# Kernel tuning notes

Measured on AMD Instinct MI355X. Metric: run time of the kernel, lower is better.

Reference implementation:

```python
import jax, jax.numpy as jnp
import numpy as np

BN_EPS = 1e-5

def _ste_sign(x):
    # forward: sign in {-1,+1}; backward: clipped straight-through (grad 1 on [-1,1])
    s = jnp.where(x >= 0, 1.0, -1.0).astype(x.dtype)
    c = jnp.clip(x, -1.0, 1.0)
    return c + jax.lax.stop_gradient(s - c)

def setup_inputs() -> dict:
    key = jax.random.key(0)
    ks = jax.random.split(key, 8)
    N, C, H, W = 32, 256, 56, 56
    x = jax.random.normal(ks[0], (N, C, H, W), dtype=jnp.float32)
    bias0 = jax.random.normal(ks[1], (C,), dtype=jnp.float32) * 0.1
    w = jax.random.normal(ks[2], (C, C, 1, 1), dtype=jnp.float32) * 0.05
    gamma = jnp.ones((C,), dtype=jnp.float32)
    beta = jnp.zeros((C,), dtype=jnp.float32)
    bias1 = jax.random.normal(ks[3], (C,), dtype=jnp.float32) * 0.1
    alpha = jnp.full((C,), 0.25, dtype=jnp.float32)  # PReLU init
    bias2 = jax.random.normal(ks[4], (C,), dtype=jnp.float32) * 0.1
    return {"x": x, "bias0": bias0, "w": w, "gamma": gamma, "beta": beta,
            "bias1": bias1, "alpha": alpha, "bias2": bias2}

def reference(x, bias0, w, gamma, beta, bias1, alpha, bias2):
    ch = lambda v: v[None, :, None, None]
    # move0: learnable per-channel bias
    out = x + ch(bias0)
    # binary activation: sign (STE)
    out = _ste_sign(out)
    # binarized 1x1 conv: w_bin = mean(|w|) per out-channel * sign(w)
    scale = jnp.mean(jnp.abs(w), axis=(1, 2, 3))              # [O]
    wb = scale[:, None] * _ste_sign(w[:, :, 0, 0])            # [O, C]
    out = jnp.einsum('nchw,oc->nohw', out, wb)                # 1x1 conv
    # bn1: batch statistics (training-mode math)
    mu = jnp.mean(out, axis=(0, 2, 3), keepdims=True)
    var = jnp.var(out, axis=(0, 2, 3), keepdims=True)
    out = ch(gamma) * (out - mu) * jax.lax.rsqrt(var + BN_EPS) + ch(beta)
    # residual add (downsample is None)
    out = out + x
    # move1 -> PReLU -> move2
    out = out + ch(bias1)
    out = jnp.where(out > 0, out, ch(alpha) * out)
    out = out + ch(bias2)
    return out
```

## Files before the change

kernel.cpp:

```cpp
#include <hip/hip_runtime.h>
#include <stdint.h>

typedef unsigned long long u64;
typedef unsigned int u32;
typedef float f32x2 __attribute__((ext_vector_type(2)));
typedef float f32x4 __attribute__((ext_vector_type(4)));

constexpr int kC  = 256;
constexpr int kHW = 3136;
constexpr int kN  = 32;
constexpr int kP  = kN * kHW;
constexpr int kPos = 128;
constexpr int kBlk = kP / kPos;
constexpr int kRedBlk  = 16;
constexpr int kRedRows = kBlk / kRedBlk;

constexpr size_t OFF_T     = 0;
constexpr size_t OFF_SCALE = 8192;
constexpr size_t OFF_SUMD  = 9216;
constexpr size_t OFF_SUMD2 = 11264;
constexpr size_t OFF_CC    = 13312;
constexpr size_t OFF_PS    = 17408;
constexpr size_t OFF_PQ    = 820224;
constexpr size_t OFF_D     = 1623040;

struct alignas(16) U64x2 { u64 x, y; };

__global__ __launch_bounds__(256) void prep_kernel(
    const float* __restrict__ w, char* __restrict__ ws) {
  int t = threadIdx.x;
  int b = blockIdx.x;
  u64*   T4    = (u64*)(ws + OFF_T);
  float* scale = (float*)(ws + OFF_SCALE);
  int kk = t >> 6, ln = t & 63;
  if (b == 0) {
    ((u64*)(ws + OFF_SUMD))[t]  = 0ull;
    ((u64*)(ws + OFF_SUMD2))[t] = 0ull;
  }
  __shared__ float part[4][16];
#pragma unroll
  for (int i = 0; i < 16; ++i) {
    int o = b * 16 + i;
    float v = w[o * kC + kk * 64 + ln];
    u64 m = __ballot(v >= 0.0f);
    float a = fabsf(v);
#pragma unroll
    for (int s = 32; s > 0; s >>= 1) a += __shfl_xor(a, s, 64);
    if (ln == 0) { T4[o * 4 + kk] = m; part[kk][i] = a; }
  }
  __syncthreads();
  if (t < 16) {
    int o = b * 16 + t;
    scale[o] = (part[0][t] + part[1][t] + part[2][t] + part[3][t]) * (1.0f / 256.0f);
  }
}

__global__ __launch_bounds__(256) void pack_d_kernel(
    const float* __restrict__ x, const float* __restrict__ bias0,
    char* __restrict__ ws) {
  __shared__ U64x2 tile[4][64];
  int t = threadIdx.x;
  int k    = __builtin_amdgcn_readfirstlane(t >> 6);
  int lane = t & 63;
  u32 pb = (u32)blockIdx.x * (u32)kPos;
  u32 p0 = pb + 2u * (u32)lane;
  u32 n  = p0 / kHW;
  u32 hw = p0 - n * kHW;
  const float* xp = x + (size_t)(n * kC + k * 64) * kHW + hw;
  const float* bp = bias0 + k * 64;

  u64 m0 = 0, m1 = 0;
#pragma unroll 8
  for (int i = 0; i < 64; ++i) {
    f32x2 v = *(const f32x2*)(xp + (size_t)i * kHW);
    float bc = bp[i];
    m0 |= (u64)(v.x + bc >= 0.0f) << i;
    m1 |= (u64)(v.y + bc >= 0.0f) << i;
  }
  U64x2 mm; mm.x = m0; mm.y = m1;
  tile[k][lane] = mm;
  __syncthreads();

  U64x2 sa = tile[0][lane], sb = tile[1][lane],
        sc = tile[2][lane], sd = tile[3][lane];

  const u64* T4 = (const u64*)(ws + OFF_T);
  u32* D = (u32*)(ws + OFF_D);
  int myPS = 0, myPQ = 0;
#pragma unroll 4
  for (int i = 0; i < 64; ++i) {
    int o = k * 64 + i;
    u64 t0 = T4[4 * o], t1 = T4[4 * o + 1], t2 = T4[4 * o + 2], t3 = T4[4 * o + 3];
    int q0 = __popcll(sa.x ^ t0) + __popcll(sb.x ^ t1) +
             __popcll(sc.x ^ t2) + __popcll(sd.x ^ t3);
    int q1 = __popcll(sa.y ^ t0) + __popcll(sb.y ^ t1) +
             __popcll(sc.y ^ t2) + __popcll(sd.y ^ t3);
    D[(size_t)o * (kP / 2) + (pb >> 1) + lane] = (u32)q0 | ((u32)q1 << 16);
    int a0 = 128 - q0, a1 = 128 - q1;
    int s  = a0 + a1;
    int sq = a0 * a0 + a1 * a1;
#pragma unroll
    for (int msk = 1; msk < 64; msk <<= 1) {
      s  += __shfl_xor(s,  msk, 64);
      sq += __shfl_xor(sq, msk, 64);
    }
    if (lane == i) { myPS = s; myPQ = sq; }
  }
  ((int*)(ws + OFF_PS))[blockIdx.x * 256 + t] = myPS;
  ((int*)(ws + OFF_PQ))[blockIdx.x * 256 + t] = myPQ;
}

__global__ __launch_bounds__(256) void reduce_kernel(char* __restrict__ ws) {
  int t = threadIdx.x;
  int b = blockIdx.x;
  const int* PS = (const int*)(ws + OFF_PS);
  const int* PQ = (const int*)(ws + OFF_PQ);
  long long s = 0, q = 0;
#pragma unroll 7
  for (int r = 0; r < kRedRows; ++r) {
    int row = b * kRedRows + r;
    s += PS[row * 256 + t];
    q += PQ[row * 256 + t];
  }
  atomicAdd((u64*)(ws + OFF_SUMD) + t,  (u64)(long long)(2 * s));
  atomicAdd((u64*)(ws + OFF_SUMD2) + t, (u64)(long long)(4 * q));
}

__global__ __launch_bounds__(256) void coef_kernel(
    const float* __restrict__ gamma, const float* __restrict__ beta,
    const float* __restrict__ bias1, const float* __restrict__ alpha,
    const float* __restrict__ bias2, char* __restrict__ ws) {
  int t = threadIdx.x;
  const float*     scale = (const float*)(ws + OFF_SCALE);
  const long long* sumd  = (const long long*)(ws + OFF_SUMD);
  const long long* sumd2 = (const long long*)(ws + OFF_SUMD2);
  double inv  = 1.0 / (double)kP;
  double md   = (double)sumd[t] * inv;
  double e2   = (double)sumd2[t] * inv;
  double vard = e2 - md * md;
  float sc  = scale[t];
  float mu  = sc * (float)md;
  float var = sc * sc * (float)vard;
  float rs  = rsqrtf(var + 1e-5f);
  float g   = gamma[t];
  float cA  = g * rs * sc;
  float cB  = beta[t] - g * rs * mu + bias1[t];
  f32x4 cc; cc.x = 2.0f * cA; cc.y = cB; cc.z = alpha[t]; cc.w = bias2[t];
  ((f32x4*)(ws + OFF_CC))[t] = cc;
}

__global__ __launch_bounds__(256) void finalize_kernel(
    const float* __restrict__ x, const char* __restrict__ ws,
    float* __restrict__ out) {
  int t = threadIdx.x;
  int k    = __builtin_amdgcn_readfirstlane(t >> 6);
  int lane = t & 63;
  u32 pb = (u32)blockIdx.x * (u32)kPos;
  u32 p0 = pb + 2u * (u32)lane;
  u32 n  = p0 / kHW;
  u32 hw = p0 - n * kHW;

  const float* xp = x   + (size_t)(n * kC + k * 64) * kHW + hw;
  float*       op = out + (size_t)(n * kC + k * 64) * kHW + hw;
  const u32*   D  = (const u32*)(ws + OFF_D);
  const f32x4* CC = (const f32x4*)(ws + OFF_CC);
  u32 dbase = (pb >> 1) + (u32)lane;

#pragma unroll 4
  for (int i = 0; i < 64; ++i) {
    int o = k * 64 + i;
    f32x4 cc = CC[o];
    u32 d = D[(size_t)o * (kP / 2) + dbase];
    f32x2 xv = *(const f32x2*)(xp + (size_t)i * kHW);
    float u0 = fmaf(cc.x, (float)(128 - (int)(d & 0xFFFFu)), cc.y) + xv.x;
    float u1 = fmaf(cc.x, (float)(128 - (int)(d >> 16)),     cc.y) + xv.y;
    f32x2 r;
    r.x = (u0 > 0.0f ? u0 : cc.z * u0) + cc.w;
    r.y = (u1 > 0.0f ? u1 : cc.z * u1) + cc.w;
    __builtin_nontemporal_store(r, (f32x2*)(op + (size_t)i * kHW));
  }
}

extern "C" void kernel_launch(void* const* d_in, const int* in_sizes, int n_in,
                              void* d_out, int out_size, void* d_ws, size_t ws_size,
                              hipStream_t stream) {
  const float* x     = (const float*)d_in[0];
  const float* bias0 = (const float*)d_in[1];
  const float* w     = (const float*)d_in[2];
  const float* gamma = (const float*)d_in[3];
  const float* beta  = (const float*)d_in[4];
  const float* bias1 = (const float*)d_in[5];
  const float* alpha = (const float*)d_in[6];
  const float* bias2 = (const float*)d_in[7];
  float* out = (float*)d_out;
  char*  ws  = (char*)d_ws;

  hipLaunchKernelGGL(prep_kernel, dim3(16), dim3(256), 0, stream, w, ws);
  hipLaunchKernelGGL(pack_d_kernel, dim3(kBlk), dim3(256), 0, stream,
                     x, bias0, ws);
  hipLaunchKernelGGL(reduce_kernel, dim3(kRedBlk), dim3(256), 0, stream, ws);
  hipLaunchKernelGGL(coef_kernel, dim3(1), dim3(256), 0, stream,
                     gamma, beta, bias1, alpha, bias2, ws);
  hipLaunchKernelGGL(finalize_kernel, dim3(kBlk), dim3(256), 0, stream,
                     x, ws, out);
}
```

Measured before the change: 273.4 us.

## Compute BN stats by rereading packed D per channel; drop shuffle reductions

```diff
diff --git a/kernel.cpp b/kernel.cpp
--- a/kernel.cpp
+++ b/kernel.cpp
@@ -12,16 +12,12 @@
 constexpr int kP  = kN * kHW;
 constexpr int kPos = 128;
 constexpr int kBlk = kP / kPos;
-constexpr int kRedBlk  = 16;
-constexpr int kRedRows = kBlk / kRedBlk;
+constexpr int kDW  = kP / 2;
+constexpr int kStIt = kDW / 256;
 
 constexpr size_t OFF_T     = 0;
 constexpr size_t OFF_SCALE = 8192;
-constexpr size_t OFF_SUMD  = 9216;
-constexpr size_t OFF_SUMD2 = 11264;
 constexpr size_t OFF_CC    = 13312;
-constexpr size_t OFF_PS    = 17408;
-constexpr size_t OFF_PQ    = 820224;
 constexpr size_t OFF_D     = 1623040;
 
 struct alignas(16) U64x2 { u64 x, y; };
@@ -33,10 +29,6 @@
   u64*   T4    = (u64*)(ws + OFF_T);
   float* scale = (float*)(ws + OFF_SCALE);
   int kk = t >> 6, ln = t & 63;
-  if (b == 0) {
-    ((u64*)(ws + OFF_SUMD))[t]  = 0ull;
-    ((u64*)(ws + OFF_SUMD2))[t] = 0ull;
-  }
   __shared__ float part[4][16];
 #pragma unroll
   for (int i = 0; i < 16; ++i) {
@@ -86,8 +78,8 @@
 
   const u64* T4 = (const u64*)(ws + OFF_T);
   u32* D = (u32*)(ws + OFF_D);
-  int myPS = 0, myPQ = 0;
-#pragma unroll 4
+  u32 dbase = (pb >> 1) + (u32)lane;
+#pragma unroll 8
   for (int i = 0; i < 64; ++i) {
     int o = k * 64 + i;
     u64 t0 = T4[4 * o], t1 = T4[4 * o + 1], t2 = T4[4 * o + 2], t3 = T4[4 * o + 3];
@@ -95,58 +87,53 @@
              __popcll(sc.x ^ t2) + __popcll(sd.x ^ t3);
     int q1 = __popcll(sa.y ^ t0) + __popcll(sb.y ^ t1) +
              __popcll(sc.y ^ t2) + __popcll(sd.y ^ t3);
-    D[(size_t)o * (kP / 2) + (pb >> 1) + lane] = (u32)q0 | ((u32)q1 << 16);
-    int a0 = 128 - q0, a1 = 128 - q1;
-    int s  = a0 + a1;
-    int sq = a0 * a0 + a1 * a1;
-#pragma unroll
-    for (int msk = 1; msk < 64; msk <<= 1) {
-      s  += __shfl_xor(s,  msk, 64);
-      sq += __shfl_xor(sq, msk, 64);
-    }
-    if (lane == i) { myPS = s; myPQ = sq; }
+    D[(size_t)o * kDW + dbase] = (u32)q0 | ((u32)q1 << 16);
   }
-  ((int*)(ws + OFF_PS))[blockIdx.x * 256 + t] = myPS;
-  ((int*)(ws + OFF_PQ))[blockIdx.x * 256 + t] = myPQ;
 }
 
-__global__ __launch_bounds__(256) void reduce_kernel(char* __restrict__ ws) {
-  int t = threadIdx.x;
-  int b = blockIdx.x;
-  const int* PS = (const int*)(ws + OFF_PS);
-  const int* PQ = (const int*)(ws + OFF_PQ);
-  long long s = 0, q = 0;
-#pragma unroll 7
-  for (int r = 0; r < kRedRows; ++r) {
-    int row = b * kRedRows + r;
-    s += PS[row * 256 + t];
-    q += PQ[row * 256 + t];
-  }
-  atomicAdd((u64*)(ws + OFF_SUMD) + t,  (u64)(long long)(2 * s));
-  atomicAdd((u64*)(ws + OFF_SUMD2) + t, (u64)(long long)(4 * q));
-}
-
-__global__ __launch_bounds__(256) void coef_kernel(
+__global__ __launch_bounds__(256) void stats_coef_kernel(
     const float* __restrict__ gamma, const float* __restrict__ beta,
     const float* __restrict__ bias1, const float* __restrict__ alpha,
     const float* __restrict__ bias2, char* __restrict__ ws) {
   int t = threadIdx.x;
-  const float*     scale = (const float*)(ws + OFF_SCALE);
-  const long long* sumd  = (const long long*)(ws + OFF_SUMD);
-  const long long* sumd2 = (const long long*)(ws + OFF_SUMD2);
-  double inv  = 1.0 / (double)kP;
-  double md   = (double)sumd[t] * inv;
-  double e2   = (double)sumd2[t] * inv;
-  double vard = e2 - md * md;
-  float sc  = scale[t];
-  float mu  = sc * (float)md;
-  float var = sc * sc * (float)vard;
-  float rs  = rsqrtf(var + 1e-5f);
-  float g   = gamma[t];
-  float cA  = g * rs * sc;
-  float cB  = beta[t] - g * rs * mu + bias1[t];
-  f32x4 cc; cc.x = 2.0f * cA; cc.y = cB; cc.z = alpha[t]; cc.w = bias2[t];
-  ((f32x4*)(ws + OFF_CC))[t] = cc;
+  int o = blockIdx.x;
+  int wid = t >> 6, lane = t & 63;
+  const u32* Do = (const u32*)(ws + OFF_D) + (size_t)o * kDW;
+
+  int s = 0, sq = 0;
+#pragma unroll 14
+  for (int j = 0; j < kStIt; ++j) {
+    u32 d = Do[j * 256 + t];
+    int a0 = 128 - (int)(d & 0xFFFFu);
+    int a1 = 128 - (int)(d >> 16);
+    s  += a0 + a1;
+    sq += a0 * a0 + a1 * a1;
+  }
+#pragma unroll
+  for (int m = 32; m > 0; m >>= 1) {
+    s  += __shfl_down(s,  m, 64);
+    sq += __shfl_down(sq, m, 64);
+  }
+  __shared__ long long wsS[4], wsQ[4];
+  if (lane == 0) { wsS[wid] = s; wsQ[wid] = sq; }
+  __syncthreads();
+  if (t == 0) {
+    long long S  = wsS[0] + wsS[1] + wsS[2] + wsS[3];
+    long long SQ = wsQ[0] + wsQ[1] + wsQ[2] + wsQ[3];
+    double inv  = 1.0 / (double)kP;
+    double md   = (double)(2ll * S) * inv;
+    double e2   = (double)(4ll * SQ) * inv;
+    double vard = e2 - md * md;
+    float sc  = ((const float*)(ws + OFF_SCALE))[o];
+    float mu  = sc * (float)md;
+    float var = sc * sc * (float)vard;
+    float rs  = rsqrtf(var + 1e-5f);
+    float g   = gamma[o];
+    float cA  = g * rs * sc;
+    float cB  = beta[o] - g * rs * mu + bias1[o];
+    f32x4 cc; cc.x = 2.0f * cA; cc.y = cB; cc.z = alpha[o]; cc.w = bias2[o];
+    ((f32x4*)(ws + OFF_CC))[o] = cc;
+  }
 }
 
 __global__ __launch_bounds__(256) void finalize_kernel(
@@ -170,7 +157,7 @@
   for (int i = 0; i < 64; ++i) {
     int o = k * 64 + i;
     f32x4 cc = CC[o];
-    u32 d = D[(size_t)o * (kP / 2) + dbase];
+    u32 d = D[(size_t)o * kDW + dbase];
     f32x2 xv = *(const f32x2*)(xp + (size_t)i * kHW);
     float u0 = fmaf(cc.x, (float)(128 - (int)(d & 0xFFFFu)), cc.y) + xv.x;
     float u1 = fmaf(cc.x, (float)(128 - (int)(d >> 16)),     cc.y) + xv.y;
@@ -198,8 +185,7 @@
   hipLaunchKernelGGL(prep_kernel, dim3(16), dim3(256), 0, stream, w, ws);
   hipLaunchKernelGGL(pack_d_kernel, dim3(kBlk), dim3(256), 0, stream,
                      x, bias0, ws);
-  hipLaunchKernelGGL(reduce_kernel, dim3(kRedBlk), dim3(256), 0, stream, ws);
-  hipLaunchKernelGGL(coef_kernel, dim3(1), dim3(256), 0, stream,
+  hipLaunchKernelGGL(stats_coef_kernel, dim3(256), dim3(256), 0, stream,
                      gamma, beta, bias1, alpha, bias2, ws);
   hipLaunchKernelGGL(finalize_kernel, dim3(kBlk), dim3(256), 0, stream,
                      x, ws, out);
```

Result: faster. 264.9 us (-3.1%).
